# Kernel tuning notes

Hardware: AMD Instinct MI355X
Metric: run time of the kernel (lower is better)

The kernel has to match this reference:

```python
import jax, jax.numpy as jnp
import numpy as np

# norse-default LIF/LI constants (RecNet overrides alpha=80, tau_mem_inv=100)
DT = 0.001
ALPHA = 80.0
TAU_SYN_INV = 200.0   # 1/5e-3 (default)
TAU_MEM_INV = 100.0   # 1/0.01 (passed explicitly)
V_TH, V_RESET, V_LEAK = 1.0, 0.0, 0.0

@jax.custom_vjp
def superspike(x):
    # heaviside forward, SuperSpike surrogate backward
    return (x > 0).astype(x.dtype)

def _ss_fwd(x):
    return (x > 0).astype(x.dtype), x

def _ss_bwd(x, g):
    return (g / (ALPHA * jnp.abs(x) + 1.0) ** 2,)

superspike.defvjp(_ss_fwd, _ss_bwd)

def setup_inputs() -> dict:
    key = jax.random.key(0)
    k1, k2, k3, k4 = jax.random.split(key, 4)
    T, B, F, H, O = 100, 512, 784, 512, 10
    x = jax.random.normal(k1, (T, B, 1, 28, 28), dtype=jnp.float32)
    w_in = jax.random.normal(k2, (H, F), dtype=jnp.float32) / np.sqrt(F)
    w_rec = jax.random.normal(k3, (H, H), dtype=jnp.float32) / np.sqrt(H)
    w_out = jax.random.normal(k4, (O, H), dtype=jnp.float32) / np.sqrt(H)
    return {"x": x, "w_in": w_in, "w_rec": w_rec, "w_out": w_out}

def reference(x, w_in, w_rec, w_out):
    T, B = x.shape[0], x.shape[1]
    Hd = w_in.shape[0]
    Od = w_out.shape[0]
    xf = x.reshape(T, B, -1)  # [T, B, F]

    z0 = jnp.zeros((B, Hd), x.dtype)
    lv0 = jnp.zeros((B, Od), x.dtype)
    init = (z0, z0, z0, lv0, lv0)  # (z, v, i, li_v, li_i)

    def step(carry, xt):
        z, v, i, lv, li = carry
        # LIF recurrent cell (norse lif_step)
        v_dec = v + DT * TAU_MEM_INV * ((V_LEAK - v) + i)
        i_dec = i - DT * TAU_SYN_INV * i
        z_new = superspike(v_dec - V_TH)
        v_new = (1.0 - z_new) * v_dec + z_new * V_RESET
        i_new = i_dec + xt @ w_in.T + z @ w_rec.T  # previous z for recurrence
        # readout linear (no bias)
        y = z_new @ w_out.T
        # LI cell (norse li_feed_forward_step): vo uses old current
        lv_new = lv + DT * TAU_MEM_INV * ((V_LEAK - lv) + li)
        li_new = li - DT * TAU_SYN_INV * li + y
        return (z_new, v_new, i_new, lv_new, li_new), lv_new

    _, voltages = jax.lax.scan(step, init, xf)
    return voltages  # [T, B, O]
```

## Files before the change

### kernel.cpp

```cpp
#include <hip/hip_runtime.h>


#define TT    100
#define BATCH 512
#define FDIM  784
#define HDIM  512
#define ODIM  10
#define NSTATE (BATCH * HDIM)

#define DTM 0.1
#define DTS 0.2

__global__ __launch_bounds__(256) void gemm_in_kernel(const float* __restrict__ A,
                                                      const float* __restrict__ B,
                                                      double* __restrict__ C) {
  __shared__ float As[16][68];
  __shared__ float Bs[16][68];
  const int tid = threadIdx.x;
  const int tn = tid & 15;
  const int tm = tid >> 4;
  const int m0 = blockIdx.x << 6;
  const int n0 = blockIdx.y << 6;
  const int lrow = tid >> 2;
  const int lkc  = (tid & 3) << 2;

  double acc[4][4] = {};

  for (int kt = 0; kt < 49; ++kt) {
    __syncthreads();
    const float4 a = *(const float4*)(A + (size_t)(m0 + lrow) * FDIM + kt * 16 + lkc);
    As[lkc + 0][lrow] = a.x; As[lkc + 1][lrow] = a.y;
    As[lkc + 2][lrow] = a.z; As[lkc + 3][lrow] = a.w;
    const float4 b = *(const float4*)(B + (size_t)(n0 + lrow) * FDIM + kt * 16 + lkc);
    Bs[lkc + 0][lrow] = b.x; Bs[lkc + 1][lrow] = b.y;
    Bs[lkc + 2][lrow] = b.z; Bs[lkc + 3][lrow] = b.w;
    __syncthreads();
#pragma unroll
    for (int kk = 0; kk < 16; ++kk) {
      const float4 af = *(const float4*)&As[kk][tm << 2];
      const float4 bf = *(const float4*)&Bs[kk][tn << 2];
      const double am[4] = {(double)af.x, (double)af.y, (double)af.z, (double)af.w};
      const double bn[4] = {(double)bf.x, (double)bf.y, (double)bf.z, (double)bf.w};
#pragma unroll
      for (int i = 0; i < 4; ++i)
#pragma unroll
        for (int j = 0; j < 4; ++j) acc[i][j] += am[i] * bn[j];
    }
  }
#pragma unroll
  for (int i = 0; i < 4; ++i) {
    double* crow = C + (size_t)(m0 + (tm << 2) + i) * HDIM + n0 + (tn << 2);
    *(double2*)(crow)     = make_double2(acc[i][0], acc[i][1]);
    *(double2*)(crow + 2) = make_double2(acc[i][2], acc[i][3]);
  }
}

__global__ __launch_bounds__(256) void transpose_kernel(const float* __restrict__ src,
                                                        float* __restrict__ dst) {
  __shared__ float tile[32][33];
  const int bx = blockIdx.x & 15, by = blockIdx.x >> 4;
  const int tx = threadIdx.x & 31, ty = threadIdx.x >> 5;
  const int x = (bx << 5) + tx;
#pragma unroll
  for (int s = 0; s < 32; s += 8)
    tile[ty + s][tx] = src[(size_t)((by << 5) + ty + s) * HDIM + x];
  __syncthreads();
  const int xo = (by << 5) + tx;
#pragma unroll
  for (int s = 0; s < 32; s += 8)
    dst[(size_t)((bx << 5) + ty + s) * HDIM + xo] = tile[tx][ty + s];
}

__global__ __launch_bounds__(256) void wot_kernel(const float* __restrict__ w_out,
                                                  float* __restrict__ wot) {
  const int k = (blockIdx.x << 8) + threadIdx.x;
#pragma unroll
  for (int o = 0; o < ODIM; ++o) wot[(k << 4) + o] = w_out[(size_t)o * HDIM + k];
}

__global__ __launch_bounds__(256) void lif_kernel(const double* __restrict__ cin,
                                                  const float* __restrict__ wrt,
                                                  const float* __restrict__ wot,
                                                  float* __restrict__ out) {
  const int b = blockIdx.x;
  const int tid = threadIdx.x;
  const int h0 = tid, h1 = tid + 256;

  __shared__ unsigned long long masks[8];
  __shared__ int offs[9];
  __shared__ __align__(8) unsigned short list[528];
  __shared__ double ypart[256];

  if (tid == 0) offs[8] = 0;
  __syncthreads();

  double v0 = 0.0, v1 = 0.0, i0 = 0.0, i1 = 0.0;
  double lv = 0.0, li = 0.0;

  const double* cinb = cin + (size_t)b * HDIM;
  float* outb = out + (size_t)b * ODIM;

  for (int t = 0; t < TT; ++t) {
    const double vd0 = v0 + DTM * ((0.0 - v0) + i0);
    const double vd1 = v1 + DTM * ((0.0 - v1) + i1);
    const bool s0 = (vd0 - 1.0) > 0.0;
    const bool s1 = (vd1 - 1.0) > 0.0;
    v0 = s0 ? 0.0 : vd0;
    v1 = s1 ? 0.0 : vd1;
    i0 = i0 - DTS * i0;
    i1 = i1 - DTS * i1;

    const double c0 = cinb[(size_t)t * NSTATE + h0];
    const double c1 = cinb[(size_t)t * NSTATE + h1];

    {
      const int nf = offs[8];
      const int nfp = (nf + 3) & ~3;
      if (nfp > 0) {
        float A0[4], A1[4], B0[4] = {}, B1[4] = {};
#define LOADG(base, X0, X1)                                                   \
        do {                                                                  \
          const unsigned long long le = *(const unsigned long long*)&list[base]; \
          const int k0 = (int)(le & 0xffffu), k1 = (int)((le >> 16) & 0xffffu); \
          const int k2 = (int)((le >> 32) & 0xffffu), k3 = (int)(le >> 48);   \
          X0[0] = wrt[(k0 << 9) + h0]; X1[0] = wrt[(k0 << 9) + h1];           \
          X0[1] = wrt[(k1 << 9) + h0]; X1[1] = wrt[(k1 << 9) + h1];           \
          X0[2] = wrt[(k2 << 9) + h0]; X1[2] = wrt[(k2 << 9) + h1];           \
          X0[3] = wrt[(k3 << 9) + h0]; X1[3] = wrt[(k3 << 9) + h1];           \
        } while (0)
        LOADG(0, A0, A1);
        for (int g = 0; g < nfp; g += 4) {
          if (g + 4 < nfp) LOADG(g + 4, B0, B1);
          i0 += (double)A0[0]; i1 += (double)A1[0];
          i0 += (double)A0[1]; i1 += (double)A1[1];
          i0 += (double)A0[2]; i1 += (double)A1[2];
          i0 += (double)A0[3]; i1 += (double)A1[3];
#pragma unroll
          for (int j = 0; j < 4; ++j) { A0[j] = B0[j]; A1[j] = B1[j]; }
        }
#undef LOADG
      }
    }
    i0 += c0;
    i1 += c1;

    __syncthreads();

    {
      const unsigned long long m0 = __ballot(s0);
      const unsigned long long m1 = __ballot(s1);
      const int w = tid >> 6;
      if ((tid & 63) == 0) { masks[w] = m0; masks[4 + w] = m1; }
    }
    __syncthreads();
    if (tid == 0) {
      int r = 0;
#pragma unroll
      for (int q = 0; q < 8; ++q) { offs[q] = r; r += __popcll(masks[q]); }
      offs[8] = r;
    }
    __syncthreads();
    if (tid < 8) {
      unsigned long long m = masks[tid];
      int o = offs[tid];
      const int base = tid << 6;
      while (m) {
        list[o++] = (unsigned short)(base + __builtin_ctzll(m));
        m &= m - 1;
      }
    }
    if (tid < 4) list[offs[8] + tid] = 512;
    __syncthreads();

    {
      const int o = tid & 15, q = tid >> 4;
      const int nfc = offs[8];
      double yp = 0.0;
      int kk = q;
      if (kk < nfc) {
        float f = wot[((int)list[kk] << 4) + o];
        for (kk += 16; kk < nfc; kk += 16) {
          const float fn = wot[((int)list[kk] << 4) + o];
          yp += (double)f;
          f = fn;
        }
        yp += (double)f;
      }
      ypart[(o << 4) + q] = yp;
    }
    __syncthreads();
    if (tid < ODIM) {
      double y = 0.0;
      const double* yr = &ypart[tid << 4];
#pragma unroll
      for (int q = 0; q < 16; ++q) y += yr[q];
      const double lvn = lv + DTM * ((0.0 - lv) + li);
      li = (li - DTS * li) + y;
      lv = lvn;
      outb[(size_t)t * (BATCH * ODIM) + tid] = (float)lvn;
    }
  }
}

extern "C" void kernel_launch(void* const* d_in, const int* in_sizes, int n_in,
                              void* d_out, int out_size, void* d_ws, size_t ws_size,
                              hipStream_t stream) {
  const float* x     = (const float*)d_in[0];
  const float* w_in  = (const float*)d_in[1];
  const float* w_rec = (const float*)d_in[2];
  const float* w_out = (const float*)d_in[3];
  float* out = (float*)d_out;

  const size_t CIN = (size_t)TT * BATCH * HDIM;
  double* cin = (double*)d_ws;
  float* wrt = (float*)(cin + CIN);
  float* wot = wrt + 513 * 512;

  const size_t aux_floats = 513ull * 512 + 513ull * 16;
  const size_t need_bytes = CIN * sizeof(double) + aux_floats * sizeof(float);
  if (ws_size < need_bytes) {
    hipMemsetAsync(d_out, 0x7F, (size_t)out_size * sizeof(float), stream);
    return;
  }

  hipMemsetAsync(wrt, 0, aux_floats * sizeof(float), stream);
  transpose_kernel<<<256, 256, 0, stream>>>(w_rec, wrt);
  wot_kernel<<<2, 256, 0, stream>>>(w_out, wot);
  gemm_in_kernel<<<dim3(800, 8), 256, 0, stream>>>(x, w_in, cin);
  lif_kernel<<<BATCH, 256, 0, stream>>>(cin, wrt, wot, out);
}
```

Baseline: 1.207 ms.

## Use FP64 MFMA for input projection GEMM with runtime lane-layout probe

Replaces the scalar FP64 FMA input GEMM with the 16x16x4 FP64 MFMA matrix instruction. Operands are staged in shared memory as doubles, and each wave computes a 32x32 sub-tile. A one-wave probe kernel works out the MFMA operand and result lane mapping at runtime and falls back to the old scalar path if none matches. The grid is also swapped so that blocks sharing an x row-tile run next to each other, which should improve reuse of x. The cost is one extra tiny kernel launch and a branch in the GEMM kernel.

```diff
diff --git a/kernel.cpp b/kernel.cpp
--- a/kernel.cpp
+++ b/kernel.cpp
@@ -11,47 +11,142 @@
 #define DTM 0.1
 #define DTS 0.2
 
+typedef double f64x4 __attribute__((ext_vector_type(4)));
+
+__device__ __forceinline__ void h_maps(int H, int lane,
+                                       int& am, int& ak, int& bn, int& bk,
+                                       int dr[4], int dc[4]) {
+  const int l15 = lane & 15, l4 = lane >> 4;
+  const int lq = lane >> 2, l3 = lane & 3;
+  if (H & 1) { am = lq;  ak = l3; } else { am = l15; ak = l4; }
+  if (H & 2) { bn = lq;  bk = l3; } else { bn = l15; bk = l4; }
+  const int dmode = H >> 2;
+#pragma unroll
+  for (int r = 0; r < 4; ++r) {
+    const int rr = (dmode & 1) ? (l4 + (r << 2)) : ((l4 << 2) + r);
+    if (dmode & 2) { dr[r] = l15; dc[r] = rr; }
+    else           { dr[r] = rr;  dc[r] = l15; }
+  }
+}
+
+__global__ __launch_bounds__(64) void probe_kernel(int* __restrict__ flag) {
+  const int lane = threadIdx.x;
+  int winner = -1;
+  for (int H = 0; H < 16; ++H) {
+    int am, ak, bn, bk, dr[4], dc[4];
+    h_maps(H, lane, am, ak, bn, bk, dr, dc);
+    bool ok = true;
+#pragma unroll
+    for (int s = 0; s < 2; ++s) {
+      const int c0 = s ? 2 : 3, c1 = s ? 13 : 7, c2 = s ? 9 : 5, c3 = s ? 4 : 11;
+      const double a = (double)(1 + c0 * am + c1 * ak);
+      const double b = (double)(1 + c2 * bn + c3 * bk);
+      f64x4 d = {0.0, 0.0, 0.0, 0.0};
+      d = __builtin_amdgcn_mfma_f64_16x16x4f64(a, b, d, 0, 0, 0);
+#pragma unroll
+      for (int r = 0; r < 4; ++r) {
+        double ref = 0.0;
+#pragma unroll
+        for (int k = 0; k < 4; ++k)
+          ref += (double)((1 + c0 * dr[r] + c1 * k) * (1 + c2 * dc[r] + c3 * k));
+        ok = ok && (d[r] == ref);
+      }
+    }
+    if (__all(ok) && winner < 0) winner = H;
+  }
+  if (lane == 0) *flag = winner;
+}
+
 __global__ __launch_bounds__(256) void gemm_in_kernel(const float* __restrict__ A,
                                                       const float* __restrict__ B,
-                                                      double* __restrict__ C) {
-  __shared__ float As[16][68];
-  __shared__ float Bs[16][68];
-  const int tid = threadIdx.x;
-  const int tn = tid & 15;
-  const int tm = tid >> 4;
-  const int m0 = blockIdx.x << 6;
-  const int n0 = blockIdx.y << 6;
-  const int lrow = tid >> 2;
-  const int lkc  = (tid & 3) << 2;
-
-  double acc[4][4] = {};
-
-  for (int kt = 0; kt < 49; ++kt) {
-    __syncthreads();
-    const float4 a = *(const float4*)(A + (size_t)(m0 + lrow) * FDIM + kt * 16 + lkc);
-    As[lkc + 0][lrow] = a.x; As[lkc + 1][lrow] = a.y;
-    As[lkc + 2][lrow] = a.z; As[lkc + 3][lrow] = a.w;
-    const float4 b = *(const float4*)(B + (size_t)(n0 + lrow) * FDIM + kt * 16 + lkc);
-    Bs[lkc + 0][lrow] = b.x; Bs[lkc + 1][lrow] = b.y;
-    Bs[lkc + 2][lrow] = b.z; Bs[lkc + 3][lrow] = b.w;
-    __syncthreads();
-#pragma unroll
-    for (int kk = 0; kk < 16; ++kk) {
-      const float4 af = *(const float4*)&As[kk][tm << 2];
-      const float4 bf = *(const float4*)&Bs[kk][tn << 2];
-      const double am[4] = {(double)af.x, (double)af.y, (double)af.z, (double)af.w};
-      const double bn[4] = {(double)bf.x, (double)bf.y, (double)bf.z, (double)bf.w};
-#pragma unroll
-      for (int i = 0; i < 4; ++i)
-#pragma unroll
-        for (int j = 0; j < 4; ++j) acc[i][j] += am[i] * bn[j];
-    }
-  }
-#pragma unroll
-  for (int i = 0; i < 4; ++i) {
-    double* crow = C + (size_t)(m0 + (tm << 2) + i) * HDIM + n0 + (tn << 2);
-    *(double2*)(crow)     = make_double2(acc[i][0], acc[i][1]);
-    *(double2*)(crow + 2) = make_double2(acc[i][2], acc[i][3]);
+                                                      double* __restrict__ C,
+                                                      const int* __restrict__ flag) {
+  __shared__ __align__(16) double Al[4][16][16];
+  __shared__ __align__(16) double Bl[4][16][16];
+  const int tid  = threadIdx.x;
+  const int lane = tid & 63;
+  const int qm   = (tid >> 6) & 1;
+  const int qn   = tid >> 7;
+  const int n0 = blockIdx.x << 6;
+  const int m0 = blockIdx.y << 6;
+  const int srow = tid >> 2;
+  const int skc  = (tid & 3) << 2;
+  const int st = srow >> 4, sr = srow & 15;
+  const int H = flag[0];
+
+  const float* Arow = A + (size_t)(m0 + srow) * FDIM + skc;
+  const float* Brow = B + (size_t)(n0 + srow) * FDIM + skc;
+
+  if (H >= 0) {
+    int am, ak, bn, bk, dr[4], dc[4];
+    h_maps(H, lane, am, ak, bn, bk, dr, dc);
+    f64x4 acc[2][2] = {};
+    for (int kt = 0; kt < 49; ++kt) {
+      __syncthreads();
+      const float4 a4 = *(const float4*)(Arow + kt * 16);
+      Al[st][skc + 0][sr] = (double)a4.x;
+      Al[st][skc + 1][sr] = (double)a4.y;
+      Al[st][skc + 2][sr] = (double)a4.z;
+      Al[st][skc + 3][sr] = (double)a4.w;
+      const float4 b4 = *(const float4*)(Brow + kt * 16);
+      Bl[st][skc + 0][sr] = (double)b4.x;
+      Bl[st][skc + 1][sr] = (double)b4.y;
+      Bl[st][skc + 2][sr] = (double)b4.z;
+      Bl[st][skc + 3][sr] = (double)b4.w;
+      __syncthreads();
+#pragma unroll
+      for (int ks = 0; ks < 4; ++ks) {
+        const double a0 = Al[(qm << 1) + 0][(ks << 2) + ak][am];
+        const double a1 = Al[(qm << 1) + 1][(ks << 2) + ak][am];
+        const double b0 = Bl[(qn << 1) + 0][(ks << 2) + bk][bn];
+        const double b1 = Bl[(qn << 1) + 1][(ks << 2) + bk][bn];
+        acc[0][0] = __builtin_amdgcn_mfma_f64_16x16x4f64(a0, b0, acc[0][0], 0, 0, 0);
+        acc[0][1] = __builtin_amdgcn_mfma_f64_16x16x4f64(a0, b1, acc[0][1], 0, 0, 0);
+        acc[1][0] = __builtin_amdgcn_mfma_f64_16x16x4f64(a1, b0, acc[1][0], 0, 0, 0);
+        acc[1][1] = __builtin_amdgcn_mfma_f64_16x16x4f64(a1, b1, acc[1][1], 0, 0, 0);
+      }
+    }
+#pragma unroll
+    for (int i = 0; i < 2; ++i)
+#pragma unroll
+      for (int j = 0; j < 2; ++j)
+#pragma unroll
+        for (int r = 0; r < 4; ++r)
+          C[(size_t)(m0 + (((qm << 1) + i) << 4) + dr[r]) * HDIM
+            + n0 + (((qn << 1) + j) << 4) + dc[r]] = acc[i][j][r];
+  } else {
+    float* Asf = (float*)&Al[0][0][0];
+    float* Bsf = (float*)&Bl[0][0][0];
+    const int tn = tid & 15, tm = tid >> 4;
+    const int lrow = tid >> 2, lkc = (tid & 3) << 2;
+    double acc[4][4] = {};
+    for (int kt = 0; kt < 49; ++kt) {
+      __syncthreads();
+      const float4 a = *(const float4*)(A + (size_t)(m0 + lrow) * FDIM + kt * 16 + lkc);
+      Asf[(lkc + 0) * 68 + lrow] = a.x; Asf[(lkc + 1) * 68 + lrow] = a.y;
+      Asf[(lkc + 2) * 68 + lrow] = a.z; Asf[(lkc + 3) * 68 + lrow] = a.w;
+      const float4 b = *(const float4*)(B + (size_t)(n0 + lrow) * FDIM + kt * 16 + lkc);
+      Bsf[(lkc + 0) * 68 + lrow] = b.x; Bsf[(lkc + 1) * 68 + lrow] = b.y;
+      Bsf[(lkc + 2) * 68 + lrow] = b.z; Bsf[(lkc + 3) * 68 + lrow] = b.w;
+      __syncthreads();
+#pragma unroll
+      for (int kk = 0; kk < 16; ++kk) {
+        const float4 af = *(const float4*)&Asf[kk * 68 + (tm << 2)];
+        const float4 bf = *(const float4*)&Bsf[kk * 68 + (tn << 2)];
+        const double amv[4] = {(double)af.x, (double)af.y, (double)af.z, (double)af.w};
+        const double bnv[4] = {(double)bf.x, (double)bf.y, (double)bf.z, (double)bf.w};
+#pragma unroll
+        for (int i = 0; i < 4; ++i)
+#pragma unroll
+          for (int j = 0; j < 4; ++j) acc[i][j] += amv[i] * bnv[j];
+      }
+    }
+#pragma unroll
+    for (int i = 0; i < 4; ++i) {
+      double* crow = C + (size_t)(m0 + (tm << 2) + i) * HDIM + n0 + (tn << 2);
+      *(double2*)(crow)     = make_double2(acc[i][0], acc[i][1]);
+      *(double2*)(crow + 2) = make_double2(acc[i][2], acc[i][3]);
+    }
   }
 }
 
@@ -215,17 +310,19 @@
   double* cin = (double*)d_ws;
   float* wrt = (float*)(cin + CIN);
   float* wot = wrt + 513 * 512;
+  int* flag  = (int*)(wot + 513 * 16);
 
   const size_t aux_floats = 513ull * 512 + 513ull * 16;
-  const size_t need_bytes = CIN * sizeof(double) + aux_floats * sizeof(float);
+  const size_t need_bytes = CIN * sizeof(double) + aux_floats * sizeof(float) + 16;
   if (ws_size < need_bytes) {
     hipMemsetAsync(d_out, 0x7F, (size_t)out_size * sizeof(float), stream);
     return;
   }
 
   hipMemsetAsync(wrt, 0, aux_floats * sizeof(float), stream);
+  probe_kernel<<<1, 64, 0, stream>>>(flag);
   transpose_kernel<<<256, 256, 0, stream>>>(w_rec, wrt);
   wot_kernel<<<2, 256, 0, stream>>>(w_out, wot);
-  gemm_in_kernel<<<dim3(800, 8), 256, 0, stream>>>(x, w_in, cin);
+  gemm_in_kernel<<<dim3(8, 800), 256, 0, stream>>>(x, w_in, cin, flag);
   lif_kernel<<<BATCH, 256, 0, stream>>>(cin, wrt, wot, out);
 }
```

New measurement: 1.192 ms. About the same (-1.3%).
